# Optimization experiments

Measured on AMD Instinct MI355X. Metric: run time of the kernel, lower is better.

## Reference

```python
import jax, jax.numpy as jnp
import numpy as np

T_MAX = 26  # hardcoded 26 char steps in the torch module

def _resize(x, hw):
    # torch F.interpolate bilinear, align_corners=False (half-pixel) == jax linear, no antialias
    return jax.image.resize(x, x.shape[:-2] + hw, method='linear', antialias=False)

def _ce(logits, labels):
    # per-element cross entropy, labels int
    logp = jax.nn.log_softmax(logits, axis=-1)
    return -jnp.take_along_axis(logp, labels[:, None].astype(jnp.int32), axis=-1)[:, 0]


def setup_inputs() -> dict:
    key = jax.random.key(0)
    ks = jax.random.split(key, 6)
    b, H, W, L = 512, 32, 128, 64
    hm, wm, hl, wl = 16, 64, 8, 32
    return {
        'masks': jax.random.uniform(ks[0], (b, 1, H, W), dtype=jnp.float32),
        'backfore_feature': jax.random.normal(ks[1], (b, 2, H, W), dtype=jnp.float32),
        'seq1_attention_map': jax.random.uniform(ks[2], (b, L, T_MAX), dtype=jnp.float32),
        'char_middle': jax.random.normal(ks[3], (b, 27, hm, wm), dtype=jnp.float32),
        'char_low': jax.random.normal(ks[4], (b, 27, hl, wl), dtype=jnp.float32),
        'length': jax.random.randint(ks[5], (b,), 2, 27),
        'iteration': 1000,
        'alpha': jnp.float32(0.1),
    }


def reference(masks, backfore_feature, seq1_attention_map, char_middle, char_low, length, iteration, alpha):
    b, _, H, W = masks.shape
    f32 = masks.dtype
    masks_i = (masks > 0.5).astype(jnp.int32)                      # [b,1,H,W]
    sm = jax.nn.softmax(backfore_feature, axis=1)                  # [b,2,H,W]

    # ---- SegLoss: CE applied to softmax probs as if logits (faithful to torch) ----
    per_elem = _ce(sm.transpose(0, 2, 3, 1).reshape(-1, 2), masks_i.reshape(-1))
    if iteration > 20000:
        value = per_elem.reshape(b, -1).mean(1)
        sel = (value < 1.0).astype(f32)
        predmask_loss = (value * sel).sum() / jnp.maximum(sel.sum(), 1.0)
    else:
        predmask_loss = per_elem.mean()

    fore_mask = (sm[:, 1] > 0.5).astype(jnp.int32)[:, None]        # [b,1,H,W], int -> no grad
    Attn = jnp.transpose(seq1_attention_map, (0, 2, 1))            # [b,26,L]
    n = length - 1                                                  # valid chars per sample
    nf = n.astype(f32)
    row_valid = (jnp.arange(T_MAX)[None, :] < n[:, None]).astype(f32)  # [b,26]

    # ---- Correct_1D_Location (seg mask detached; Attn gets grads) ----
    fore_d = jax.lax.stop_gradient(fore_mask)
    interp = _resize(Attn[:, None], (T_MAX, W))[:, 0]              # [b,26,W]
    # pairwise sum_{i<j} sum_w (v_i v_j)^2 over the first n rows, vectorized
    sq = jnp.square(interp) * row_valid[:, :, None]
    S = sq.sum(1)
    S2 = jnp.square(sq).sum(1)
    irrelevant = (0.5 * (jnp.square(S) - S2).sum(-1) / nf).sum()
    act = jax.nn.sigmoid(70.0 * (interp - 0.1)) * row_valid[:, :, None]
    # sum_t act[t,w] * mask[h,w] == (sum_t act)[w] * mask[h,w]
    char_sum = jnp.clip(act.sum(1)[:, None, :] * fore_d[:, 0].astype(f32), 0.0, 1.0)  # [b,H,W]
    single2 = jnp.stack([1.0 - char_sum, char_sum], axis=-1)       # [b,H,W,2]
    correct_loss = _ce(single2.reshape(-1, 2), fore_d.reshape(-1)).mean() + irrelevant

    # ---- Char_Segmention_Loss (attention and fore mask detached) ----
    attn_clr = jax.lax.stop_gradient(Attn) * row_valid[:, :, None]  # clear_noise

    def char_branch(char_feat):
        h, w = char_feat.shape[2], char_feat.shape[3]
        fm = (_resize(fore_d.astype(f32), (h, w)) >= 0.4).astype(jnp.int32)   # [b,1,h,w]
        ai = _resize(attn_clr[:, None], (T_MAX, w))[:, 0]
        ab = (ai > alpha).astype(jnp.int32)                                   # [b,26,w]
        single = ab[:, :, None, :] * fm                                       # [b,26,h,w]
        mask27 = jnp.concatenate([1 - fm, single], axis=1)                    # [b,27,h,w]
        labels = jnp.argmax(mask27, axis=1).reshape(-1)
        cel = _ce(char_feat.transpose(0, 2, 3, 1).reshape(-1, 27), labels).mean()
        soft = jax.nn.softmax(char_feat, axis=1)
        m1 = soft[:, 1:].reshape(b, T_MAX, -1)
        m2 = mask27[:, 1:].astype(f32).reshape(b, T_MAX, -1)
        inter = (m1 * m2).sum(-1)
        score = (2.0 * inter + 1.0) / (m1.sum(-1) + m2.sum(-1) + 1.0)         # [b,26]
        dice = (((1.0 - score) * row_valid).sum(-1) / nf).sum() / b
        return cel + dice, mask27, soft

    loss_middle, _, soft_mid = char_branch(char_middle)
    loss_low, mask_low, soft_low = char_branch(char_low)

    return (predmask_loss, correct_loss, loss_low, loss_middle,
            mask_low, soft_mid[:, 1:], soft_low[:, 1:])
```

## Files before the change

kernel.cpp:

```cpp
#include <hip/hip_runtime.h>
#include <math.h>

#define NB 512
#define TT 26
#define LL 64
#define HH 32
#define WW 128

typedef unsigned long long ull;

__device__ __forceinline__ float wave_sum(float v) {
#pragma unroll
  for (int o = 32; o > 0; o >>= 1) v += __shfl_xor(v, o, 64);
  return v;
}

template<int CTRL, int RM>
__device__ __forceinline__ float dpp_add(float x) {
  int y = __builtin_amdgcn_update_dpp(0, __float_as_int(x), CTRL, RM, 0xf, true);
  return x + __int_as_float(y);
}
__device__ __forceinline__ float wave_red63(float x) {
  x = dpp_add<0x111, 0xf>(x);
  x = dpp_add<0x112, 0xf>(x);
  x = dpp_add<0x114, 0xf>(x);
  x = dpp_add<0x118, 0xf>(x);
  x = dpp_add<0x142, 0xa>(x);
  x = dpp_add<0x143, 0xc>(x);
  return x;
}


__global__ __launch_bounds__(1024) void k_mega(
    const float* __restrict__ masks, const float* __restrict__ bf,
    const float* __restrict__ seq, const float* __restrict__ cm,
    const float* __restrict__ cl, const int* __restrict__ length,
    const float* __restrict__ alpha_p,
    float* __restrict__ out_mask, float* __restrict__ out_smid,
    float* __restrict__ out_slow, float* __restrict__ perb)
{
  int b = blockIdx.x;
  int tid = threadIdx.x;
  int lane = tid & 63, wv = tid >> 6;

  __shared__ float att[LL * TT];
  __shared__ float wsA_lds[WW];
  __shared__ ull s_bits[TT];
  __shared__ unsigned s_alow[TT];
  __shared__ unsigned s_cols_mid[64];
  __shared__ unsigned s_cols_low[32];
  __shared__ ull fmsk_lds[64];
  __shared__ ull s_fmrow[16];
  __shared__ unsigned fmrow32[8];
  __shared__ float s_red_in[16][TT], s_red_m1[16][TT];
  __shared__ float s_ce[16];
  __shared__ float ps[16], pc[16];
  __shared__ float wpart[2];
  __shared__ float s_dice[TT];

  int n = length[b] - 1;
  float alpha = alpha_p[0];
  float inv_n = 1.f / (float)n;

  const float* sb = seq + (size_t)b * (LL * TT);
  for (int i = tid; i < LL * TT; i += 1024) att[i] = sb[i];
  __syncthreads();

  if (tid < 128) {
    int w = tid;
    int k = w >> 1;
    int i0, i1; float c0, c1;
    if ((w & 1) == 0) {
      if (k == 0) { i0 = 0; i1 = 0; c0 = 1.f; c1 = 0.f; }
      else        { i0 = k - 1; i1 = k; c0 = 0.25f; c1 = 0.75f; }
    } else {
      if (k == 63) { i0 = 63; i1 = 63; c0 = 1.f; c1 = 0.f; }
      else         { i0 = k; i1 = k + 1; c0 = 0.75f; c1 = 0.25f; }
    }
    float S = 0.f, S2 = 0.f, A = 0.f;
    for (int t = 0; t < n; ++t) {
      float v = c0 * att[i0 * TT + t] + c1 * att[i1 * TT + t];
      float s = v * v;
      S += s; S2 += s * s;
      A += 1.f / (1.f + __expf(-70.f * (v - 0.1f)));
    }
    wsA_lds[w] = A;
    float c = S * S - S2;
    c = wave_sum(c);
    if (lane == 0) wpart[wv] = c;
  }
  if (tid < 64) {
    int x = tid;
    for (int t = 0; t < TT; ++t) {
      bool pred = (t < n) && (att[x * TT + t] > alpha);
      ull m = __ballot(pred);
      if (x == 0) s_bits[t] = m;
    }
  } else if (tid < 128) {
    int x = tid - 64;
    for (int t = 0; t < TT; ++t) {
      bool pred = (x < 32) && (t < n) &&
                  (0.5f * (att[(2 * x) * TT + t] + att[(2 * x + 1) * TT + t]) > alpha);
      ull m = __ballot(pred);
      if (x == 0) s_alow[t] = (unsigned)m;
    }
  }
  __syncthreads();
  if (tid == 0) perb[b * 8 + 2] = 0.5f * (wpart[0] + wpart[1]) * inv_n;

  if (tid < 64) {
    unsigned cb = 0;
#pragma unroll
    for (int t = 0; t < TT; ++t) cb |= (unsigned)((s_bits[t] >> tid) & 1ULL) << t;
    s_cols_mid[tid] = cb;
  } else if (tid < 96) {
    int xc = tid - 64;
    unsigned cb = 0;
#pragma unroll
    for (int t = 0; t < TT; ++t) cb |= ((s_alow[t] >> xc) & 1u) << t;
    s_cols_low[xc] = cb;
  }

  {
    const float* mb = masks + (size_t)b * 4096;
    const float* fb = bf + (size_t)b * 8192;
    float A = wsA_lds[tid & 127];
    float cs = fminf(fmaxf(A, 0.f), 1.f);
    float ce_fore = log1pf(__expf(1.f - 2.f * cs));
    float seg_acc = 0.f, cor_acc = 0.f;
    for (int k = 0; k < 4; ++k) {
      int px = k * 1024 + tid;
      float m = mb[px];
      float b0 = fb[px];
      float b1 = fb[4096 + px];
      float mx = fmaxf(b0, b1);
      float e0 = __expf(b0 - mx), e1 = __expf(b1 - mx);
      float inv = 1.f / (e0 + e1);
      float p0 = e0 * inv, p1 = e1 * inv;
      float pm = fmaxf(p0, p1);
      float lse = pm + log1pf(__expf(-fabsf(p1 - p0)));
      seg_acc += lse - ((m > 0.5f) ? p1 : p0);
      bool fore = b1 > b0;
      cor_acc += fore ? ce_fore : 0.313261687518222834f;
      ull fbm = __ballot(fore);
      if (lane == 0) fmsk_lds[k * 16 + wv] = fbm;
    }
    seg_acc = wave_red63(seg_acc);
    cor_acc = wave_red63(cor_acc);
    if (lane == 63) { ps[wv] = seg_acc; pc[wv] = cor_acc; }
  }
  __syncthreads();
  if (tid == 0) {
    float s = 0.f, c = 0.f;
#pragma unroll
    for (int i = 0; i < 16; ++i) { s += ps[i]; c += pc[i]; }
    perb[b * 8 + 0] = s;
    perb[b * 8 + 1] = c;
  }

  {
    int y = wv;
    int x = tid & 63;
    int word = x >> 5;
    int p = (x & 31) * 2;
    ull r0 = fmsk_lds[4 * y + word];
    ull r1 = fmsk_lds[4 * y + 2 + word];
    int cnt = (int)((r0 >> p) & 1) + (int)((r0 >> (p + 1)) & 1)
            + (int)((r1 >> p) & 1) + (int)((r1 >> (p + 1)) & 1);
    bool fm = cnt >= 2;
    unsigned cbk = s_cols_mid[x];
    int lab = (fm && cbk) ? __ffs((int)cbk) : 0;
    if (!fm) cbk = 0;
    ull bmv = __ballot(fm);
    if (lane == 0) s_fmrow[wv] = bmv;

    const float* base = cm + (size_t)b * 27 * 1024 + tid;
    float v[27];
    float xl = 0.f, s0 = 0.f;
#pragma unroll
    for (int c = 0; c < 27; ++c) {
      float r = base[(size_t)c * 1024];
      xl = (c == lab) ? r : xl;
      r = __expf(r);
      v[c] = r;
      s0 += r;
    }
    float inv0 = 1.f / s0;
    float ce_part = __logf(s0) - xl;

    float* os = out_smid + (size_t)b * 26 * 1024 + tid;
#pragma unroll
    for (int t = 0; t < TT; ++t) {
      float m1 = v[t + 1] * inv0;
      os[(size_t)t * 1024] = m1;
      float ri = wave_red63(((cbk >> t) & 1) ? m1 : 0.f);
      float rm = wave_red63(m1);
      if (lane == 63) { s_red_in[wv][t] = ri; s_red_m1[wv][t] = rm; }
    }
    float rce = wave_red63(ce_part);
    if (lane == 63) s_ce[wv] = rce;
  }
  __syncthreads();
  if (tid < TT) {
    float m2v = 0.f;
#pragma unroll
    for (int r = 0; r < 16; ++r) m2v += (float)__popcll(s_fmrow[r] & s_bits[tid]);
    float si = 0.f, sm = 0.f;
#pragma unroll
    for (int w = 0; w < 16; ++w) { si += s_red_in[w][tid]; sm += s_red_m1[w][tid]; }
    float sc = (2.f * si + 1.f) / (sm + m2v + 1.f);
    s_dice[tid] = (tid < n) ? (1.f - sc) * inv_n : 0.f;
  }
  if (tid == TT) {
    float c16 = 0.f;
#pragma unroll
    for (int w = 0; w < 16; ++w) c16 += s_ce[w];
    perb[b * 8 + 3] = c16;
  }
  __syncthreads();
  if (tid == 0) {
    float dm = 0.f;
#pragma unroll
    for (int t = 0; t < TT; ++t) dm += s_dice[t];
    perb[b * 8 + 5] = dm;
  }

  if (tid < 256) {
    int px = tid;
    int y = px >> 5, x = px & 31;
    int wb = 4 * x + 1;
    int word = wb >> 6;
    int p = wb & 63;
    ull r0 = fmsk_lds[(4 * y + 1) * 2 + word];
    ull r1 = fmsk_lds[(4 * y + 2) * 2 + word];
    int cnt = (int)((r0 >> p) & 1) + (int)((r0 >> (p + 1)) & 1)
            + (int)((r1 >> p) & 1) + (int)((r1 >> (p + 1)) & 1);
    bool fm = cnt >= 2;
    unsigned cbk = s_cols_low[x];
    int lab = (fm && cbk) ? __ffs((int)cbk) : 0;
    if (!fm) cbk = 0;
    ull bmv = __ballot(fm);
    if (lane == 0) {
      fmrow32[2 * wv] = (unsigned)bmv;
      fmrow32[2 * wv + 1] = (unsigned)(bmv >> 32);
    }

    const float* base = cl + (size_t)b * 27 * 256 + px;
    float v[27];
    float xl = 0.f, s0 = 0.f;
#pragma unroll
    for (int c = 0; c < 27; ++c) {
      float r = base[(size_t)c * 256];
      xl = (c == lab) ? r : xl;
      r = __expf(r);
      v[c] = r;
      s0 += r;
    }
    float inv0 = 1.f / s0;
    float ce_part = __logf(s0) - xl;

    float* om  = out_mask + (size_t)b * 27 * 256 + px;
    float* osf = out_slow + (size_t)b * 26 * 256 + px;
    om[0] = fm ? 0.f : 1.f;
#pragma unroll
    for (int t = 0; t < TT; ++t) {
      float m1 = v[t + 1] * inv0;
      osf[(size_t)t * 256] = m1;
      bool m2 = (cbk >> t) & 1;
      om[(size_t)(t + 1) * 256] = m2 ? 1.f : 0.f;
      float ri = wave_red63(m2 ? m1 : 0.f);
      float rm = wave_red63(m1);
      if (lane == 63) { s_red_in[wv][t] = ri; s_red_m1[wv][t] = rm; }
    }
    float rce = wave_red63(ce_part);
    if (lane == 63) s_ce[wv] = rce;
  }
  __syncthreads();
  if (tid < TT) {
    float m2v = 0.f;
#pragma unroll
    for (int yy = 0; yy < 8; ++yy) m2v += (float)__popc(fmrow32[yy] & s_alow[tid]);
    float si = 0.f, sm = 0.f;
#pragma unroll
    for (int w = 0; w < 4; ++w) { si += s_red_in[w][tid]; sm += s_red_m1[w][tid]; }
    float sc = (2.f * si + 1.f) / (sm + m2v + 1.f);
    s_dice[tid] = (tid < n) ? (1.f - sc) * inv_n : 0.f;
  }
  if (tid == TT) perb[b * 8 + 4] = s_ce[0] + s_ce[1] + s_ce[2] + s_ce[3];
  __syncthreads();
  if (tid == 0) {
    float dl = 0.f;
#pragma unroll
    for (int t = 0; t < TT; ++t) dl += s_dice[t];
    perb[b * 8 + 6] = dl;
  }
}

__global__ __launch_bounds__(512) void k_final(
    const float* __restrict__ perb, const int* __restrict__ iter_p,
    float* __restrict__ out)
{
  int tid = threadIdx.x;
  const float4* pb4 = (const float4*)perb;
  float4 p0 = pb4[2 * tid];
  float4 p1 = pb4[2 * tid + 1];
  float seg = p0.x, cor = p0.y, irr = p0.z, celm = p0.w;
  float cell = p1.x, dm = p1.y, dl = p1.z;

  float val = seg * (1.f / 4096.f);
  float sel = (val < 1.f) ? 1.f : 0.f;
  float ssel = (val < 1.f) ? val : 0.f;

  float q[9] = {seg, cor, irr, celm, cell, dm, dl, sel, ssel};
  __shared__ float red[9][8];
  int lane = tid & 63, wv = tid >> 6;
#pragma unroll
  for (int j = 0; j < 9; ++j) {
    float r = wave_sum(q[j]);
    if (lane == 0) red[j][wv] = r;
  }
  __syncthreads();
  if (tid == 0) {
    float a[9];
#pragma unroll
    for (int j = 0; j < 9; ++j) {
      float s = 0.f;
      for (int i = 0; i < 8; ++i) s += red[j][i];
      a[j] = s;
    }
    float pred = (iter_p[0] > 20000) ? (a[8] / fmaxf(a[7], 1.f)) : (a[0] / 2097152.f);
    out[0] = pred;
    out[1] = a[1] / 2097152.f + a[2];
    out[2] = a[4] / 131072.f + a[6] / 512.f;
    out[3] = a[3] / 524288.f + a[5] / 512.f;
  }
}

extern "C" void kernel_launch(void* const* d_in, const int* in_sizes, int n_in,
                              void* d_out, int out_size, void* d_ws, size_t ws_size,
                              hipStream_t stream) {
  (void)in_sizes; (void)n_in; (void)out_size; (void)ws_size;
  const float* masks  = (const float*)d_in[0];
  const float* bf     = (const float*)d_in[1];
  const float* seq    = (const float*)d_in[2];
  const float* cmid   = (const float*)d_in[3];
  const float* clow   = (const float*)d_in[4];
  const int*   length = (const int*)d_in[5];
  const int*   iter   = (const int*)d_in[6];
  const float* alpha  = (const float*)d_in[7];
  float* out = (float*)d_out;

  float* perb = (float*)d_ws;

  float* out_mask = out + 4;
  float* out_smid = out + 4 + 3538944;
  float* out_slow = out + 4 + 3538944 + 13631488;

  k_mega<<<NB, 1024, 0, stream>>>(masks, bf, seq, cmid, clow, length, alpha,
                                  out_mask, out_smid, out_slow, perb);
  k_final<<<1, 512, 0, stream>>>(perb, iter, out);
}
```

Before: 55.00 us.

## Prefetch inputs early and stage char_middle channels into LDS asynchronously

```diff
diff --git a/kernel.cpp b/kernel.cpp
--- a/kernel.cpp
+++ b/kernel.cpp
@@ -28,6 +28,18 @@
   x = dpp_add<0x142, 0xa>(x);
   x = dpp_add<0x143, 0xc>(x);
   return x;
+}
+
+__device__ __forceinline__ void gload_lds16(const float* g, float* l) {
+  __builtin_amdgcn_global_load_lds(
+      (__attribute__((address_space(1))) void*)(g),
+      (__attribute__((address_space(3))) void*)(l), 16, 0, 0);
+}
+
+__device__ __forceinline__ void barrier_lgkm() {
+  asm volatile("s_waitcnt lgkmcnt(0)" ::: "memory");
+  __builtin_amdgcn_s_barrier();
+  __builtin_amdgcn_sched_barrier(0);
 }
 
 
@@ -43,6 +55,7 @@
   int tid = threadIdx.x;
   int lane = tid & 63, wv = tid >> 6;
 
+  __shared__ float cmbuf[16 * 1024];
   __shared__ float att[LL * TT];
   __shared__ float wsA_lds[WW];
   __shared__ ull s_bits[TT];
@@ -63,8 +76,29 @@
   float inv_n = 1.f / (float)n;
 
   const float* sb = seq + (size_t)b * (LL * TT);
-  for (int i = tid; i < LL * TT; i += 1024) att[i] = sb[i];
-  __syncthreads();
+  float a0 = sb[tid];
+  float a1 = (tid < LL * TT - 1024) ? sb[1024 + tid] : 0.f;
+
+  const float* mb = masks + (size_t)b * 4096;
+  const float* fbp = bf + (size_t)b * 8192;
+  float m_r[4], b0_r[4], b1_r[4];
+#pragma unroll
+  for (int k = 0; k < 4; ++k) {
+    m_r[k]  = mb[k * 1024 + tid];
+    b0_r[k] = fbp[k * 1024 + tid];
+    b1_r[k] = fbp[4096 + k * 1024 + tid];
+  }
+
+  {
+    const float* cm_base = cm + (size_t)b * 27648 + (size_t)wv * 1024;
+#pragma unroll
+    for (int i = 0; i < 4; ++i)
+      gload_lds16(cm_base + i * 256 + lane * 4, cmbuf + wv * 1024 + i * 256);
+  }
+
+  att[tid] = a0;
+  if (tid < LL * TT - 1024) att[1024 + tid] = a1;
+  barrier_lgkm();
 
   if (tid < 128) {
     int w = tid;
@@ -105,7 +139,7 @@
       if (x == 0) s_alow[t] = (unsigned)m;
     }
   }
-  __syncthreads();
+  barrier_lgkm();
   if (tid == 0) perb[b * 8 + 2] = 0.5f * (wpart[0] + wpart[1]) * inv_n;
 
   if (tid < 64) {
@@ -122,17 +156,15 @@
   }
 
   {
-    const float* mb = masks + (size_t)b * 4096;
-    const float* fb = bf + (size_t)b * 8192;
     float A = wsA_lds[tid & 127];
     float cs = fminf(fmaxf(A, 0.f), 1.f);
     float ce_fore = log1pf(__expf(1.f - 2.f * cs));
     float seg_acc = 0.f, cor_acc = 0.f;
+#pragma unroll
     for (int k = 0; k < 4; ++k) {
-      int px = k * 1024 + tid;
-      float m = mb[px];
-      float b0 = fb[px];
-      float b1 = fb[4096 + px];
+      float m = m_r[k];
+      float b0 = b0_r[k];
+      float b1 = b1_r[k];
       float mx = fmaxf(b0, b1);
       float e0 = __expf(b0 - mx), e1 = __expf(b1 - mx);
       float inv = 1.f / (e0 + e1);
@@ -179,7 +211,7 @@
     float xl = 0.f, s0 = 0.f;
 #pragma unroll
     for (int c = 0; c < 27; ++c) {
-      float r = base[(size_t)c * 1024];
+      float r = (c < 16) ? cmbuf[c * 1024 + tid] : base[(size_t)c * 1024];
       xl = (c == lab) ? r : xl;
       r = __expf(r);
       v[c] = r;
```

Measured after the change: 58.58 us. +6.5%, slower.
